# Kernel tuning notes

Hardware: AMD Instinct MI355X
Metric: run time of the kernel (lower is better)

Reference implementation:

```python
import jax, jax.numpy as jnp
import numpy as np

DIM = 4096
K = 16  # 2**bits, bits=4
SCALE = 1.0 / DIM ** 0.5
# Lloyd-Max optimal 16-level quantizer centroids for N(0,1)
LLOYD_MAX_4BIT = np.array([
    -2.7326, -2.0690, -1.6181, -1.2562, -0.9424, -0.6568, -0.3881, -0.1284,
     0.1284,  0.3881,  0.6568,  0.9424,  1.2562,  1.6181,  2.0690,  2.7326,
], dtype=np.float32)


def setup_inputs() -> dict:
    key = jax.random.key(0)
    k_x, k_q = jax.random.split(key)
    x = jax.random.normal(k_x, (2048, DIM), dtype=jnp.float32)
    # Random orthogonal rotation via QR, matching torch.linalg.qr(randn(dim, dim))
    g = jax.random.normal(k_q, (DIM, DIM), dtype=jnp.float32)
    rotation, _ = jnp.linalg.qr(g)
    codebook = jnp.asarray(LLOYD_MAX_4BIT)
    return {"x": x, "rotation": rotation, "codebook": codebook}


def reference(x, rotation, codebook):
    # x: (N, dim); rotation: (dim, dim) orthogonal; codebook: (K,)
    shape = x.shape
    x_flat = x.reshape(-1, DIM).astype(jnp.float32)
    y = x_flat @ rotation.T                      # (N, dim) rotate
    y_norm = y / SCALE                           # coords ~ N(0, 1)
    # (N, dim, K) distance tensor -> argmin over codebook axis
    dists = jnp.abs(y_norm[..., None] - codebook)
    idx = jnp.argmin(dists, axis=-1)             # (N, dim) int32
    y_hat = codebook[idx] * SCALE                # gather + rescale
    x_hat = y_hat @ rotation                     # inverse rotation
    return x_hat.reshape(shape)
```

## Files before the change

### kernel.cpp

```cpp
#include <hip/hip_runtime.h>
#include <hip/hip_bf16.h>


typedef __attribute__((ext_vector_type(8))) _Float16 f16x8;
typedef __attribute__((ext_vector_type(4))) float f32x4;

__device__ __forceinline__ unsigned short f2h(float f) {
    _Float16 h = (_Float16)f;
    return *reinterpret_cast<unsigned short*>(&h);
}

__global__ __launch_bounds__(256) void convert_x_kernel(
    const float* __restrict__ x, unsigned short* __restrict__ xb) {
    const int i = (blockIdx.x * 256 + threadIdx.x) * 4;
    float4 v = *reinterpret_cast<const float4*>(x + i);
    ushort4 b;
    b.x = f2h(v.x); b.y = f2h(v.y); b.z = f2h(v.z); b.w = f2h(v.w);
    *reinterpret_cast<ushort4*>(xb + i) = b;
}

__global__ __launch_bounds__(256) void conv_rot_kernel(
    const float* __restrict__ R, unsigned short* __restrict__ Rb,
    unsigned short* __restrict__ Rt) {
    __shared__ float t[64][65];
    const int tid = threadIdx.x;
    const int tr = blockIdx.y * 64, tc = blockIdx.x * 64;
    const int r0 = tid >> 4;
    const int c4 = (tid & 15) << 2;
#pragma unroll
    for (int i = 0; i < 4; i++) {
        const int r = r0 + i * 16;
        float4 v = *reinterpret_cast<const float4*>(
            &R[(size_t)(tr + r) * 4096 + tc + c4]);
        ushort4 b;
        b.x = f2h(v.x); b.y = f2h(v.y); b.z = f2h(v.z); b.w = f2h(v.w);
        *reinterpret_cast<ushort4*>(&Rb[(size_t)(tr + r) * 4096 + tc + c4]) = b;
        t[r][c4 + 0] = v.x; t[r][c4 + 1] = v.y;
        t[r][c4 + 2] = v.z; t[r][c4 + 3] = v.w;
    }
    __syncthreads();
#pragma unroll
    for (int i = 0; i < 16; i++) {
        const int idx = tid + 256 * i;
        const int rr = idx >> 6;
        const int cc = idx & 63;
        Rt[(size_t)(tc + rr) * 4096 + tr + cc] = f2h(t[cc][rr]);
    }
}

constexpr int GK = 4096;
constexpr int BM = 128, BN = 256, BK = 32;
constexpr int NT = GK / BK;
constexpr int A_LDS = BM * BK * 2;
constexpr int BUF = (BM + BN) * BK * 2;
constexpr int LDS_DYN = 3 * BUF;

template <bool QUANT>
__global__ __launch_bounds__(512, 4) void gemm_nt_kernel(
    const unsigned short* __restrict__ A, const unsigned short* __restrict__ Bt,
    void* __restrict__ Cout, const float* __restrict__ cb16) {
    extern __shared__ char smem[];
    const int tid = threadIdx.x;
    const int lane = tid & 63;
    const int w = tid >> 6;
    const int wm = w >> 2;
    const int wn = w & 3;

    const int bid = blockIdx.x;
    const int wgid = (bid & 7) * 32 + (bid >> 3);
    const int tn = wgid & 15;
    const int tm = wgid >> 4;

    f32x4 acc[4][4];
#pragma unroll
    for (int m = 0; m < 4; m++)
#pragma unroll
        for (int n = 0; n < 4; n++) acc[m][n] = (f32x4){0.f, 0.f, 0.f, 0.f};

    const int srow = tid >> 2;
    const int scol = (((tid & 3) ^ ((srow >> 1) & 3)) << 3);
    const unsigned short* ApS = A + (size_t)(tm * BM + srow) * GK + scol;
    const unsigned short* BpS0 = Bt + (size_t)(tn * BN + srow) * GK + scol;
    const unsigned short* BpS1 = BpS0 + (size_t)128 * GK;
    const int wbase = (w << 10);

#define STAGE(dstbase)                                                         \
    {                                                                          \
        __builtin_amdgcn_global_load_lds(                                      \
            (const __attribute__((address_space(1))) void*)ApS,                \
            (__attribute__((address_space(3))) void*)(smem + (dstbase) + wbase), 16, 0, 0); \
        __builtin_amdgcn_global_load_lds(                                      \
            (const __attribute__((address_space(1))) void*)BpS0,               \
            (__attribute__((address_space(3))) void*)(smem + (dstbase) + A_LDS + wbase), 16, 0, 0); \
        __builtin_amdgcn_global_load_lds(                                      \
            (const __attribute__((address_space(1))) void*)BpS1,               \
            (__attribute__((address_space(3))) void*)(smem + (dstbase) + A_LDS + 8192 + wbase), 16, 0, 0); \
        ApS += BK; BpS0 += BK; BpS1 += BK;                                     \
    }

    const int sw = (((lane >> 4) ^ (((lane & 15) >> 1) & 3)) << 4);
    const int arow = (wm * 64 + (lane & 15)) * 64;
    const int brow = A_LDS + (wn * 64 + (lane & 15)) * 64;

#define LDA(m) (*reinterpret_cast<const f16x8*>(smem + lb + arow + (m) * 1024 + sw))
#define LDB(n) (*reinterpret_cast<const f16x8*>(smem + lb + brow + (n) * 1024 + sw))
#define MFMA_ROW(aR, r)                                                          \
    acc[r][0] = __builtin_amdgcn_mfma_f32_16x16x32_f16(aR, b0, acc[r][0], 0, 0, 0); \
    acc[r][1] = __builtin_amdgcn_mfma_f32_16x16x32_f16(aR, b1, acc[r][1], 0, 0, 0); \
    acc[r][2] = __builtin_amdgcn_mfma_f32_16x16x32_f16(aR, b2, acc[r][2], 0, 0, 0); \
    acc[r][3] = __builtin_amdgcn_mfma_f32_16x16x32_f16(aR, b3, acc[r][3], 0, 0, 0);

    STAGE(0)
    STAGE(BUF)
    asm volatile("s_waitcnt vmcnt(3)" ::: "memory");
    __builtin_amdgcn_s_barrier();
    __builtin_amdgcn_sched_barrier(0);

    int lb = 0;
    int wb = 2 * BUF;
    for (int t = 0; t < NT; ++t) {
        f16x8 a0, a1, a2, a3, b0, b1, b2, b3;
        a0 = LDA(0); a1 = LDA(1); a2 = LDA(2); a3 = LDA(3);
        b0 = LDB(0); b1 = LDB(1); b2 = LDB(2); b3 = LDB(3);
        if (t + 2 < NT) STAGE(wb)
        asm volatile("s_waitcnt lgkmcnt(0)" ::: "memory");
        __builtin_amdgcn_sched_barrier(0);
        __builtin_amdgcn_s_setprio(1);
        MFMA_ROW(a0, 0) MFMA_ROW(a1, 1) MFMA_ROW(a2, 2) MFMA_ROW(a3, 3)
        __builtin_amdgcn_s_setprio(0);
        if (t + 1 < NT) {
            if (t + 2 < NT) {
                asm volatile("s_waitcnt vmcnt(3)" ::: "memory");
            } else {
                asm volatile("s_waitcnt vmcnt(0)" ::: "memory");
            }
            __builtin_amdgcn_s_barrier();
            __builtin_amdgcn_sched_barrier(0);
            lb = (lb == 2 * BUF) ? 0 : lb + BUF;
            wb = (wb == 2 * BUF) ? 0 : wb + BUF;
        }
    }
#undef LDA
#undef LDB
#undef MFMA_ROW
#undef STAGE

    const int crow0 = tm * BM + wm * 64 + ((lane >> 4) << 2);
    const int ccol0 = tn * BN + wn * 64 + (lane & 15);
    if constexpr (QUANT) {
        float c[16];
#pragma unroll
        for (int i = 0; i < 16; i++) c[i] = cb16[i];
        unsigned short* O = (unsigned short*)Cout;
#pragma unroll
        for (int m = 0; m < 4; m++)
#pragma unroll
            for (int n = 0; n < 4; n++)
#pragma unroll
                for (int j = 0; j < 4; j++) {
                    const float yn = acc[m][n][j] * 64.0f;
                    float v = c[0];
#pragma unroll
                    for (int i = 0; i < 15; i++) {
                        const float bnd = 0.5f * (c[i] + c[i + 1]);
                        v = (yn > bnd) ? c[i + 1] : v;
                    }
                    O[(size_t)(crow0 + m * 16 + j) * 4096 + ccol0 + n * 16] =
                        f2h(v * 0.015625f);
                }
    } else {
        float* O = (float*)Cout;
#pragma unroll
        for (int m = 0; m < 4; m++)
#pragma unroll
            for (int n = 0; n < 4; n++)
#pragma unroll
                for (int j = 0; j < 4; j++)
                    O[(size_t)(crow0 + m * 16 + j) * 4096 + ccol0 + n * 16] =
                        acc[m][n][j];
    }
}

extern "C" void kernel_launch(void* const* d_in, const int* in_sizes, int n_in,
                              void* d_out, int out_size, void* d_ws,
                              size_t ws_size, hipStream_t stream) {
    const float* x = (const float*)d_in[0];
    const float* rot = (const float*)d_in[1];
    const float* cb = (const float*)d_in[2];
    float* out = (float*)d_out;

    unsigned short* Xh = (unsigned short*)d_ws;
    unsigned short* Rh = Xh + (size_t)2048 * 4096;
    unsigned short* Rt = Rh + (size_t)4096 * 4096;
    unsigned short* Yh = Rt + (size_t)4096 * 4096;

    (void)hipFuncSetAttribute(
        reinterpret_cast<const void*>(&gemm_nt_kernel<true>),
        hipFuncAttributeMaxDynamicSharedMemorySize, LDS_DYN);
    (void)hipFuncSetAttribute(
        reinterpret_cast<const void*>(&gemm_nt_kernel<false>),
        hipFuncAttributeMaxDynamicSharedMemorySize, LDS_DYN);

    convert_x_kernel<<<8192, 256, 0, stream>>>(x, Xh);
    conv_rot_kernel<<<dim3(64, 64), 256, 0, stream>>>(rot, Rh, Rt);
    gemm_nt_kernel<true><<<256, 512, LDS_DYN, stream>>>(Xh, Rh, (void*)Yh, cb);
    gemm_nt_kernel<false><<<256, 512, LDS_DYN, stream>>>(Yh, Rt, (void*)out, nullptr);
}
```

Measured before the change: 176.4 us.

## Add producer warps for global-to-LDS loads with double-buffered BK=64 tiles

Splits each GEMM block into 8 MFMA consumer waves and 4 dedicated producer waves that stream A/B tiles into LDS with global_load_lds, using a 2-stage double buffer with BK doubled to 64 instead of a 3-stage BK=32 ring. Consumer waves now only do LDS reads and MFMAs, with a new XOR swizzle for the wider rows, and sync with the producers through block barriers. This aims to hide load latency and halve the barrier count per K step. The cost is the extra 256 threads per block, a shallower prefetch depth, and producer waves that wait on vmcnt(0) every step, which could stall the pipeline.

```diff
diff --git a/kernel.cpp b/kernel.cpp
--- a/kernel.cpp
+++ b/kernel.cpp
@@ -8,6 +8,16 @@
 __device__ __forceinline__ unsigned short f2h(float f) {
     _Float16 h = (_Float16)f;
     return *reinterpret_cast<unsigned short*>(&h);
+}
+
+__device__ __forceinline__ float quant16(float yn, const float* c) {
+    float v = c[0];
+#pragma unroll
+    for (int i = 0; i < 15; i++) {
+        const float bnd = 0.5f * (c[i] + c[i + 1]);
+        v = (yn > bnd) ? c[i + 1] : v;
+    }
+    return v;
 }
 
 __global__ __launch_bounds__(256) void convert_x_kernel(
@@ -49,104 +59,136 @@
 }
 
 constexpr int GK = 4096;
-constexpr int BM = 128, BN = 256, BK = 32;
+constexpr int BM = 128, BN = 256, BK = 64;
 constexpr int NT = GK / BK;
 constexpr int A_LDS = BM * BK * 2;
 constexpr int BUF = (BM + BN) * BK * 2;
-constexpr int LDS_DYN = 3 * BUF;
+constexpr int LDS_DYN = 2 * BUF;
 
 template <bool QUANT>
-__global__ __launch_bounds__(512, 4) void gemm_nt_kernel(
+__global__ __launch_bounds__(768, 3) void gemm_nt_kernel(
     const unsigned short* __restrict__ A, const unsigned short* __restrict__ Bt,
     void* __restrict__ Cout, const float* __restrict__ cb16) {
     extern __shared__ char smem[];
     const int tid = threadIdx.x;
     const int lane = tid & 63;
     const int w = tid >> 6;
-    const int wm = w >> 2;
-    const int wn = w & 3;
 
     const int bid = blockIdx.x;
     const int wgid = (bid & 7) * 32 + (bid >> 3);
     const int tn = wgid & 15;
     const int tm = wgid >> 4;
 
+    if (w >= 8) {
+        const int tp = tid - 512;
+        const int pw = tp >> 6;
+        const int prow = tp >> 3;
+        const int pcol = (((tp & 7) ^ (prow & 7)) << 3);
+        const unsigned short* P[12];
+#pragma unroll
+        for (int r = 0; r < 12; r++) {
+            const int rir = r * 32 + prow;
+            P[r] = (rir < BM)
+                ? A + (size_t)(tm * BM + rir) * GK + pcol
+                : Bt + (size_t)(tn * BN + (rir - BM)) * GK + pcol;
+        }
+#pragma unroll
+        for (int r = 0; r < 12; r++) {
+            __builtin_amdgcn_global_load_lds(
+                (const __attribute__((address_space(1))) void*)P[r],
+                (__attribute__((address_space(3))) void*)(
+                    smem + r * 4096 + pw * 1024), 16, 0, 0);
+            P[r] += BK;
+        }
+        asm volatile("s_waitcnt vmcnt(0)" ::: "memory");
+        __builtin_amdgcn_s_barrier();
+        __builtin_amdgcn_sched_barrier(0);
+        int wb = BUF;
+        for (int t = 0; t < NT; ++t) {
+            if (t + 1 < NT) {
+#pragma unroll
+                for (int r = 0; r < 12; r++) {
+                    __builtin_amdgcn_global_load_lds(
+                        (const __attribute__((address_space(1))) void*)P[r],
+                        (__attribute__((address_space(3))) void*)(
+                            smem + wb + r * 4096 + pw * 1024), 16, 0, 0);
+                    P[r] += BK;
+                }
+            }
+            asm volatile("s_waitcnt vmcnt(0)" ::: "memory");
+            __builtin_amdgcn_s_barrier();
+            __builtin_amdgcn_sched_barrier(0);
+            wb ^= BUF;
+        }
+        return;
+    }
+
+    const int wm = w >> 2;
+    const int wn = w & 3;
+
     f32x4 acc[4][4];
 #pragma unroll
     for (int m = 0; m < 4; m++)
 #pragma unroll
         for (int n = 0; n < 4; n++) acc[m][n] = (f32x4){0.f, 0.f, 0.f, 0.f};
 
-    const int srow = tid >> 2;
-    const int scol = (((tid & 3) ^ ((srow >> 1) & 3)) << 3);
-    const unsigned short* ApS = A + (size_t)(tm * BM + srow) * GK + scol;
-    const unsigned short* BpS0 = Bt + (size_t)(tn * BN + srow) * GK + scol;
-    const unsigned short* BpS1 = BpS0 + (size_t)128 * GK;
-    const int wbase = (w << 10);
-
-#define STAGE(dstbase)                                                         \
-    {                                                                          \
-        __builtin_amdgcn_global_load_lds(                                      \
-            (const __attribute__((address_space(1))) void*)ApS,                \
-            (__attribute__((address_space(3))) void*)(smem + (dstbase) + wbase), 16, 0, 0); \
-        __builtin_amdgcn_global_load_lds(                                      \
-            (const __attribute__((address_space(1))) void*)BpS0,               \
-            (__attribute__((address_space(3))) void*)(smem + (dstbase) + A_LDS + wbase), 16, 0, 0); \
-        __builtin_amdgcn_global_load_lds(                                      \
-            (const __attribute__((address_space(1))) void*)BpS1,               \
-            (__attribute__((address_space(3))) void*)(smem + (dstbase) + A_LDS + 8192 + wbase), 16, 0, 0); \
-        ApS += BK; BpS0 += BK; BpS1 += BK;                                     \
-    }
-
-    const int sw = (((lane >> 4) ^ (((lane & 15) >> 1) & 3)) << 4);
-    const int arow = (wm * 64 + (lane & 15)) * 64;
-    const int brow = A_LDS + (wn * 64 + (lane & 15)) * 64;
-
-#define LDA(m) (*reinterpret_cast<const f16x8*>(smem + lb + arow + (m) * 1024 + sw))
-#define LDB(n) (*reinterpret_cast<const f16x8*>(smem + lb + brow + (n) * 1024 + sw))
-#define MFMA_ROW(aR, r)                                                          \
-    acc[r][0] = __builtin_amdgcn_mfma_f32_16x16x32_f16(aR, b0, acc[r][0], 0, 0, 0); \
-    acc[r][1] = __builtin_amdgcn_mfma_f32_16x16x32_f16(aR, b1, acc[r][1], 0, 0, 0); \
-    acc[r][2] = __builtin_amdgcn_mfma_f32_16x16x32_f16(aR, b2, acc[r][2], 0, 0, 0); \
-    acc[r][3] = __builtin_amdgcn_mfma_f32_16x16x32_f16(aR, b3, acc[r][3], 0, 0, 0);
-
-    STAGE(0)
-    STAGE(BUF)
-    asm volatile("s_waitcnt vmcnt(3)" ::: "memory");
+    const int frow = lane & 15;
+    const int sw0 = (((lane >> 4) ^ (frow & 7)) << 4);
+    const int sw1 = (((4 + (lane >> 4)) ^ (frow & 7)) << 4);
+    const int arow = (wm * 64 + frow) * 128;
+    const int brow = A_LDS + (wn * 64 + frow) * 128;
+
+#define LDA(m, sw) (*reinterpret_cast<const f16x8*>(smem + lb + arow + (m) * 2048 + (sw)))
+#define LDB(n, sw) (*reinterpret_cast<const f16x8*>(smem + lb + brow + (n) * 2048 + (sw)))
+#define MFMA16(A0, A1, A2, A3, B0, B1, B2, B3)                                     \
+    acc[0][0] = __builtin_amdgcn_mfma_f32_16x16x32_f16(A0, B0, acc[0][0], 0, 0, 0); \
+    acc[0][1] = __builtin_amdgcn_mfma_f32_16x16x32_f16(A0, B1, acc[0][1], 0, 0, 0); \
+    acc[0][2] = __builtin_amdgcn_mfma_f32_16x16x32_f16(A0, B2, acc[0][2], 0, 0, 0); \
+    acc[0][3] = __builtin_amdgcn_mfma_f32_16x16x32_f16(A0, B3, acc[0][3], 0, 0, 0); \
+    acc[1][0] = __builtin_amdgcn_mfma_f32_16x16x32_f16(A1, B0, acc[1][0], 0, 0, 0); \
+    acc[1][1] = __builtin_amdgcn_mfma_f32_16x16x32_f16(A1, B1, acc[1][1], 0, 0, 0); \
+    acc[1][2] = __builtin_amdgcn_mfma_f32_16x16x32_f16(A1, B2, acc[1][2], 0, 0, 0); \
+    acc[1][3] = __builtin_amdgcn_mfma_f32_16x16x32_f16(A1, B3, acc[1][3], 0, 0, 0); \
+    acc[2][0] = __builtin_amdgcn_mfma_f32_16x16x32_f16(A2, B0, acc[2][0], 0, 0, 0); \
+    acc[2][1] = __builtin_amdgcn_mfma_f32_16x16x32_f16(A2, B1, acc[2][1], 0, 0, 0); \
+    acc[2][2] = __builtin_amdgcn_mfma_f32_16x16x32_f16(A2, B2, acc[2][2], 0, 0, 0); \
+    acc[2][3] = __builtin_amdgcn_mfma_f32_16x16x32_f16(A2, B3, acc[2][3], 0, 0, 0); \
+    acc[3][0] = __builtin_amdgcn_mfma_f32_16x16x32_f16(A3, B0, acc[3][0], 0, 0, 0); \
+    acc[3][1] = __builtin_amdgcn_mfma_f32_16x16x32_f16(A3, B1, acc[3][1], 0, 0, 0); \
+    acc[3][2] = __builtin_amdgcn_mfma_f32_16x16x32_f16(A3, B2, acc[3][2], 0, 0, 0); \
+    acc[3][3] = __builtin_amdgcn_mfma_f32_16x16x32_f16(A3, B3, acc[3][3], 0, 0, 0);
+
     __builtin_amdgcn_s_barrier();
     __builtin_amdgcn_sched_barrier(0);
 
     int lb = 0;
-    int wb = 2 * BUF;
     for (int t = 0; t < NT; ++t) {
-        f16x8 a0, a1, a2, a3, b0, b1, b2, b3;
-        a0 = LDA(0); a1 = LDA(1); a2 = LDA(2); a3 = LDA(3);
-        b0 = LDB(0); b1 = LDB(1); b2 = LDB(2); b3 = LDB(3);
-        if (t + 2 < NT) STAGE(wb)
+        f16x8 a00, a01, a02, a03, b00, b01, b02, b03;
+        f16x8 a10, a11, a12, a13, b10, b11, b12, b13;
+        a00 = LDA(0, sw0); a01 = LDA(1, sw0); a02 = LDA(2, sw0); a03 = LDA(3, sw0);
+        b00 = LDB(0, sw0); b01 = LDB(1, sw0); b02 = LDB(2, sw0); b03 = LDB(3, sw0);
+        a10 = LDA(0, sw1); a11 = LDA(1, sw1); a12 = LDA(2, sw1); a13 = LDA(3, sw1);
+        b10 = LDB(0, sw1); b11 = LDB(1, sw1); b12 = LDB(2, sw1); b13 = LDB(3, sw1);
+        asm volatile("s_waitcnt lgkmcnt(8)" ::: "memory");
+        __builtin_amdgcn_sched_barrier(0);
+        __builtin_amdgcn_s_setprio(1);
+        MFMA16(a00, a01, a02, a03, b00, b01, b02, b03)
+        __builtin_amdgcn_s_setprio(0);
         asm volatile("s_waitcnt lgkmcnt(0)" ::: "memory");
         __builtin_amdgcn_sched_barrier(0);
         __builtin_amdgcn_s_setprio(1);
-        MFMA_ROW(a0, 0) MFMA_ROW(a1, 1) MFMA_ROW(a2, 2) MFMA_ROW(a3, 3)
+        MFMA16(a10, a11, a12, a13, b10, b11, b12, b13)
         __builtin_amdgcn_s_setprio(0);
-        if (t + 1 < NT) {
-            if (t + 2 < NT) {
-                asm volatile("s_waitcnt vmcnt(3)" ::: "memory");
-            } else {
-                asm volatile("s_waitcnt vmcnt(0)" ::: "memory");
-            }
-            __builtin_amdgcn_s_barrier();
-            __builtin_amdgcn_sched_barrier(0);
-            lb = (lb == 2 * BUF) ? 0 : lb + BUF;
-            wb = (wb == 2 * BUF) ? 0 : wb + BUF;
-        }
+        __builtin_amdgcn_s_barrier();
+        __builtin_amdgcn_sched_barrier(0);
+        lb ^= BUF;
     }
 #undef LDA
 #undef LDB
-#undef MFMA_ROW
-#undef STAGE
+#undef MFMA16
 
     const int crow0 = tm * BM + wm * 64 + ((lane >> 4) << 2);
-    const int ccol0 = tn * BN + wn * 64 + (lane & 15);
+    const int ccol0 = tn * BN + wn * 64 + frow;
     if constexpr (QUANT) {
         float c[16];
 #pragma unroll
@@ -157,17 +199,9 @@
 #pragma unroll
             for (int n = 0; n < 4; n++)
 #pragma unroll
-                for (int j = 0; j < 4; j++) {
-                    const float yn = acc[m][n][j] * 64.0f;
-                    float v = c[0];
-#pragma unroll
-                    for (int i = 0; i < 15; i++) {
-                        const float bnd = 0.5f * (c[i] + c[i + 1]);
-                        v = (yn > bnd) ? c[i + 1] : v;
-                    }
+                for (int j = 0; j < 4; j++)
                     O[(size_t)(crow0 + m * 16 + j) * 4096 + ccol0 + n * 16] =
-                        f2h(v * 0.015625f);
-                }
+                        f2h(quant16(acc[m][n][j] * 64.0f, c) * 0.015625f);
     } else {
         float* O = (float*)Cout;
 #pragma unroll
@@ -203,6 +237,6 @@
 
     convert_x_kernel<<<8192, 256, 0, stream>>>(x, Xh);
     conv_rot_kernel<<<dim3(64, 64), 256, 0, stream>>>(rot, Rh, Rt);
-    gemm_nt_kernel<true><<<256, 512, LDS_DYN, stream>>>(Xh, Rh, (void*)Yh, cb);
-    gemm_nt_kernel<false><<<256, 512, LDS_DYN, stream>>>(Yh, Rt, (void*)out, nullptr);
-}
+    gemm_nt_kernel<true><<<256, 768, LDS_DYN, stream>>>(Xh, Rh, (void*)Yh, cb);
+    gemm_nt_kernel<false><<<256, 768, LDS_DYN, stream>>>(Yh, Rt, (void*)out, nullptr);
+}
```

After: 170.0 us. 3.6% less time.
